# Optimization experiments

Hardware: AMD Instinct MI355X
Metric: run time of the kernel (lower is better)

The kernel has to match this reference:

```python
import math
import jax, jax.numpy as jnp
import numpy as np

B, I, G, C, D = 8192, 512, 32, 16, 32  # batch, dim_input, groups, num_components, dim_output
CD = C * D


def setup_inputs() -> dict:
    key = jax.random.key(0)
    ks = jax.random.split(key, 8)
    bound = 1.0 / math.sqrt(I)

    def unif(k, shape):
        return jax.random.uniform(k, shape, jnp.float32, -bound, bound)

    x = jax.random.normal(ks[0], (B, I), jnp.float32)
    # soft group-mixture weights (rows sum to 1, as produced upstream)
    g = jax.nn.softmax(jax.random.normal(ks[1], (B, G), jnp.float32), axis=-1)
    return {
        "x": x,
        "g": g,
        "W_mu": unif(ks[2], (G, I, CD)),
        "b_mu": unif(ks[3], (G, CD)),
        "W_sigma": unif(ks[4], (G, I, CD)),
        "b_sigma": unif(ks[5], (G, CD)),
        "W_pi": unif(ks[6], (G, I, C)),
        "b_pi": unif(ks[7], (G, C)),
    }


def _group_linear(x, g, W, b):
    # Fused form of: w_b = (g @ W.reshape(G, I*O)).reshape(B, I, O); x[:,None,:] @ w_b + g @ b
    # einsum avoids materializing the [B, I, O] per-sample weight tensor.
    return jnp.einsum("bi,gio,bg->bo", x, W, g) + g @ b


def reference(x, g, W_mu, b_mu, W_sigma, b_sigma, W_pi, b_pi):
    logits = _group_linear(x, g, W_pi, b_pi)                      # [B, C]
    loc = _group_linear(x, g, W_mu, b_mu)                         # [B, C*D]
    scale = jax.nn.softplus(_group_linear(x, g, W_sigma, b_sigma)) + 1e-7  # [B, C*D]
    # GroupGMM returns a MixtureSameFamily parameterized by (logits, loc, scale);
    # we return the concatenated parameter tensor [B, C + 2*C*D].
    return jnp.concatenate([logits, loc, scale], axis=-1)
```

## Files before the change

### kernel.cpp

```cpp
#include <hip/hip_runtime.h>
#include <hip/hip_bf16.h>

#define BATCH 8192
#define IDIM  512
#define GDIM  32
#define NOUT  1040
#define NPAD  1152
#define KW    16384
#define BM    128
#define BN    128
#define KQ    128

typedef short bf16x8 __attribute__((ext_vector_type(8)));
typedef float floatx4 __attribute__((ext_vector_type(4)));

__device__ inline unsigned pk2(float a, float b) {
    union { __hip_bfloat162 h2; unsigned u; } cv;
    cv.h2 = __float22bfloat162_rn(float2{a, b});
    return cv.u;
}

__global__ void cvt_bf16(const float* __restrict__ s, unsigned short* __restrict__ d) {
    int t = blockIdx.x * 256 + threadIdx.x;
    const float4* sp = (const float4*)s + (size_t)t * 2;
    float4 a = sp[0], b = sp[1];
    uint4 p;
    p.x = pk2(a.x, a.y); p.y = pk2(a.z, a.w);
    p.z = pk2(b.x, b.y); p.w = pk2(b.z, b.w);
    *(uint4*)(d + (size_t)t * 8) = p;
}

__global__ void prep_wt(const float* __restrict__ Wmu, const float* __restrict__ Wsig,
                        const float* __restrict__ Wpi, unsigned short* __restrict__ Wt) {
    int n = blockIdx.y * 256 + threadIdx.x;
    if (n >= NPAD) return;
    int k0 = blockIdx.x * 8;
    float v[8];
#pragma unroll
    for (int j = 0; j < 8; ++j) {
        int k = k0 + j, gg = k >> 9, i = k & 511;
        float val = 0.0f;
        if (n < 16)         val = Wpi [(gg * 512 + i) * 16  + n];
        else if (n < 528)   val = Wmu [(gg * 512 + i) * 512 + (n - 16)];
        else if (n < NOUT)  val = Wsig[(gg * 512 + i) * 512 + (n - 528)];
        v[j] = val;
    }
    uint4 p;
    p.x = pk2(v[0], v[1]); p.y = pk2(v[2], v[3]);
    p.z = pk2(v[4], v[5]); p.w = pk2(v[6], v[7]);
    const int col = n >> 7, r = n & 127;
    const int h = r >> 6, tn = (r >> 4) & 3, l15 = r & 15;
    const int kk = k0 >> 5, q = (k0 >> 3) & 3;
    size_t idx = ((size_t)(col * 512 + kk) << 12) + ((((h * 4 + tn) * 4 + q) * 16 + l15) * 8);
    *(uint4*)&Wt[idx] = p;
}

__global__ void prep_wb(const float* __restrict__ bmu, const float* __restrict__ bsig,
                        const float* __restrict__ bpi, unsigned short* __restrict__ Wb) {
    int n = blockIdx.y * 256 + threadIdx.x;
    if (n >= NPAD) return;
    int k0 = blockIdx.x * 8;
    float v[8];
#pragma unroll
    for (int j = 0; j < 8; ++j) {
        int gg = k0 + j;
        float val = 0.0f;
        if (n < 16)         val = bpi [gg * 16  + n];
        else if (n < 528)   val = bmu [gg * 512 + (n - 16)];
        else if (n < NOUT)  val = bsig[gg * 512 + (n - 528)];
        v[j] = val;
    }
    uint4 p;
    p.x = pk2(v[0], v[1]); p.y = pk2(v[2], v[3]);
    p.z = pk2(v[4], v[5]); p.w = pk2(v[6], v[7]);
    *(uint4*)&Wb[(size_t)n * GDIM + k0] = p;
}

__global__ __launch_bounds__(256, 2) void gemm_gmm(
        const unsigned short* __restrict__ xb, const unsigned short* __restrict__ gb,
        const float* __restrict__ g, const unsigned short* __restrict__ Wt,
        const unsigned short* __restrict__ Wb, float* __restrict__ out) {
    __shared__ unsigned short lA[BM * KQ];
    __shared__ float ratL[GDIM * BM];
    __shared__ float g31L[BM];

    const int t = threadIdx.x, lane = t & 63, w = t >> 6;
    const int wm = (w & 1) * 64, wn = (w >> 1) * 64;
    const int q = lane >> 4, l15 = lane & 15;

    const int bx = blockIdx.x;
    const int seq = (bx & 7) * 72 + (bx >> 3);
    const int col = seq >> 6, mblk = seq & 63;
    const int m0 = mblk * BM, n0 = col * BN;

    const unsigned short* Bbase = Wt + ((size_t)col * 512 << 12)
                                + (((wn >> 6) * 256 + lane) * 8);

    floatx4 acc[4][4] = {};
    uint4 breg[4][4];
    floatx4 r4[4];
    const int swA = l15 & 7;

    auto loadB = [&](int kk, int slot) {
        const unsigned kg = (((kk >> 2) & 31) * 16) + ((kk >> 7) * 4) + (kk & 3);
        const unsigned short* p = Bbase + ((size_t)kg << 12);
#pragma unroll
        for (int tn = 0; tn < 4; ++tn)
            breg[slot][tn] = *(const uint4*)(p + tn * 512);
    };
    auto loadR = [&](int gg) {
#pragma unroll
        for (int tm = 0; tm < 4; ++tm)
            r4[tm] = *(const floatx4*)&ratL[gg * BM + wm + tm * 16 + q * 4];
    };

    loadB(0, 0); loadB(1, 1); loadB(2, 2);

#pragma unroll
    for (int j = 0; j < 16; ++j) {
        int idx = t + 256 * j;
        int gg = idx >> 7, row = idx & 127;
        float cur  = g[(size_t)(m0 + row) * GDIM + gg];
        float prev = g[(size_t)(m0 + row) * GDIM + ((gg + 31) & 31)];
        ratL[idx] = prev / cur;
    }
    if (t < BM) g31L[t] = g[(size_t)(m0 + t) * GDIM + 31];
    __syncthreads();
    loadR(0);

    for (int kb = 0; kb < 4; ++kb) {
        __syncthreads();
        {
            const int r = t >> 1;
            const unsigned short* src = xb + (size_t)(m0 + r) * IDIM + kb * KQ + (t & 1) * 64;
#pragma unroll
            for (int j = 0; j < 8; ++j) {
                int gi = (t & 1) * 8 + j;
                uint4 v = *(const uint4*)(src + j * 8);
                *(uint4*)&lA[(r * 16 + (gi ^ (r & 7))) * 8] = v;
            }
        }
        __syncthreads();

        for (int gg = 0; gg < GDIM; ++gg) {
#pragma unroll
            for (int tm = 0; tm < 4; ++tm)
#pragma unroll
                for (int tn = 0; tn < 4; ++tn)
#pragma unroll
                    for (int r = 0; r < 4; ++r)
                        acc[tm][tn][r] *= r4[tm][r];
            loadR((gg + 1) & 31);

#pragma unroll
            for (int ks = 0; ks < 4; ++ks) {
                const int kk = ((kb * GDIM + gg) << 2) + ks;
                if (kk + 3 < 512) loadB(kk + 3, (ks + 3) & 3);
                bf16x8 af[4];
#pragma unroll
                for (int tm = 0; tm < 4; ++tm)
                    af[tm] = *(const bf16x8*)
                        &lA[((wm + tm * 16 + l15) * 16 + ((ks * 4 + q) ^ swA)) * 8];
#pragma unroll
                for (int tm = 0; tm < 4; ++tm)
#pragma unroll
                    for (int tn = 0; tn < 4; ++tn)
                        acc[tm][tn] = __builtin_amdgcn_mfma_f32_16x16x32_bf16(
                            af[tm], *(const bf16x8*)&breg[ks][tn], acc[tm][tn], 0, 0, 0);
            }
        }
    }

#pragma unroll
    for (int tm = 0; tm < 4; ++tm) {
        floatx4 gl = *(const floatx4*)&g31L[wm + tm * 16 + q * 4];
#pragma unroll
        for (int tn = 0; tn < 4; ++tn)
#pragma unroll
            for (int r = 0; r < 4; ++r)
                acc[tm][tn][r] *= gl[r];
    }

    __syncthreads();
    {
        const int r = t >> 1;
        const unsigned short* src = gb + (size_t)(m0 + r) * GDIM + (t & 1) * 16;
        *(uint4*)&lA[r * 40 + (t & 1) * 16]     = *(const uint4*)(src);
        *(uint4*)&lA[r * 40 + (t & 1) * 16 + 8] = *(const uint4*)(src + 8);
    }
    __syncthreads();
    {
        bf16x8 afb[4], bb[4];
#pragma unroll
        for (int tm = 0; tm < 4; ++tm)
            afb[tm] = *(const bf16x8*)&lA[(wm + tm * 16 + l15) * 40 + q * 8];
#pragma unroll
        for (int tn = 0; tn < 4; ++tn)
            bb[tn] = *(const bf16x8*)(Wb + (size_t)(n0 + wn + tn * 16 + l15) * GDIM + q * 8);
#pragma unroll
        for (int tm = 0; tm < 4; ++tm)
#pragma unroll
            for (int tn = 0; tn < 4; ++tn)
                acc[tm][tn] = __builtin_amdgcn_mfma_f32_16x16x32_bf16(
                    afb[tm], bb[tn], acc[tm][tn], 0, 0, 0);
    }

#pragma unroll
    for (int tn = 0; tn < 4; ++tn) {
        int n = n0 + wn + tn * 16 + l15;
        if (n >= NOUT) continue;
        bool is_scale = (n >= 528);
#pragma unroll
        for (int tm = 0; tm < 4; ++tm) {
            int mbase = m0 + wm + tm * 16 + q * 4;
#pragma unroll
            for (int r = 0; r < 4; ++r) {
                float vv = acc[tm][tn][r];
                if (is_scale) {
                    float sp = (vv > 15.0f) ? vv : log1pf(expf(vv));
                    vv = sp + 1e-7f;
                }
                out[(size_t)(mbase + r) * NOUT + n] = vv;
            }
        }
    }
}

extern "C" void kernel_launch(void* const* d_in, const int* in_sizes, int n_in,
                              void* d_out, int out_size, void* d_ws, size_t ws_size,
                              hipStream_t stream) {
    const float* x    = (const float*)d_in[0];
    const float* g    = (const float*)d_in[1];
    const float* Wmu  = (const float*)d_in[2];
    const float* bmu  = (const float*)d_in[3];
    const float* Wsig = (const float*)d_in[4];
    const float* bsig = (const float*)d_in[5];
    const float* Wpi  = (const float*)d_in[6];
    const float* bpi  = (const float*)d_in[7];
    float* out = (float*)d_out;

    char* ws = (char*)d_ws;
    unsigned short* Wt = (unsigned short*)ws;  ws += (size_t)NPAD * KW * 2;
    unsigned short* xb = (unsigned short*)ws;  ws += (size_t)BATCH * IDIM * 2;
    unsigned short* gb = (unsigned short*)ws;  ws += (size_t)BATCH * GDIM * 2;
    unsigned short* Wb = (unsigned short*)ws;

    cvt_bf16<<<BATCH * IDIM / 2048, 256, 0, stream>>>(x, xb);
    cvt_bf16<<<BATCH * GDIM / 2048, 256, 0, stream>>>(g, gb);
    prep_wt<<<dim3(KW / 8, 5), 256, 0, stream>>>(Wmu, Wsig, Wpi, Wt);
    prep_wb<<<dim3(GDIM / 8, 5), 256, 0, stream>>>(bmu, bsig, bpi, Wb);
    gemm_gmm<<<(BATCH / BM) * (NPAD / BN), 256, 0, stream>>>(xb, gb, g, Wt, Wb, out);
}
```

Measured before the change: 509.0 us.

## Hoist A fragments out of group loop and prefetch B per column

The A-operand fragments for all four k-steps are now loaded from LDS once per kb block into registers, instead of being reloaded every group iteration, so the same x tile is reused across all 32 groups. The B prefetch changes from a three-slot rolling buffer indexed by k-step to a per-column scheme: after each column's MFMAs finish, the next group's B fragments for that column are loaded. This removes repeated LDS reads but holds 16 more vector registers for A. The B prefetch distance also shrinks to within one group, which may expose global load latency or raise register pressure.

```diff
diff --git a/kernel.cpp b/kernel.cpp
--- a/kernel.cpp
+++ b/kernel.cpp
@@ -98,15 +98,16 @@
 
     floatx4 acc[4][4] = {};
     uint4 breg[4][4];
+    bf16x8 af[4][4];
     floatx4 r4[4];
     const int swA = l15 & 7;
 
-    auto loadB = [&](int kk, int slot) {
-        const unsigned kg = (((kk >> 2) & 31) * 16) + ((kk >> 7) * 4) + (kk & 3);
-        const unsigned short* p = Bbase + ((size_t)kg << 12);
-#pragma unroll
-        for (int tn = 0; tn < 4; ++tn)
-            breg[slot][tn] = *(const uint4*)(p + tn * 512);
+    auto loadBcol = [&](int flat, int tn) {
+        const int ggv = flat & 31, kbv = flat >> 5;
+        const unsigned short* p = Bbase + ((size_t)(ggv * 16 + kbv * 4) << 12) + tn * 512;
+#pragma unroll
+        for (int ks = 0; ks < 4; ++ks)
+            breg[ks][tn] = *(const uint4*)(p + (ks << 12));
     };
     auto loadR = [&](int gg) {
 #pragma unroll
@@ -114,7 +115,8 @@
             r4[tm] = *(const floatx4*)&ratL[gg * BM + wm + tm * 16 + q * 4];
     };
 
-    loadB(0, 0); loadB(1, 1); loadB(2, 2);
+#pragma unroll
+    for (int tn = 0; tn < 4; ++tn) loadBcol(0, tn);
 
 #pragma unroll
     for (int j = 0; j < 16; ++j) {
@@ -142,32 +144,30 @@
         }
         __syncthreads();
 
+#pragma unroll
+        for (int ks = 0; ks < 4; ++ks)
+#pragma unroll
+            for (int tm = 0; tm < 4; ++tm)
+                af[ks][tm] = *(const bf16x8*)
+                    &lA[((wm + tm * 16 + l15) * 16 + ((ks * 4 + q) ^ swA)) * 8];
+
         for (int gg = 0; gg < GDIM; ++gg) {
-#pragma unroll
-            for (int tm = 0; tm < 4; ++tm)
-#pragma unroll
-                for (int tn = 0; tn < 4; ++tn)
+            const int flat = kb * GDIM + gg;
+#pragma unroll
+            for (int tn = 0; tn < 4; ++tn) {
+#pragma unroll
+                for (int tm = 0; tm < 4; ++tm) {
 #pragma unroll
                     for (int r = 0; r < 4; ++r)
                         acc[tm][tn][r] *= r4[tm][r];
+#pragma unroll
+                    for (int ks = 0; ks < 4; ++ks)
+                        acc[tm][tn] = __builtin_amdgcn_mfma_f32_16x16x32_bf16(
+                            af[ks][tm], *(const bf16x8*)&breg[ks][tn], acc[tm][tn], 0, 0, 0);
+                }
+                if (flat + 1 < 128) loadBcol(flat + 1, tn);
+            }
             loadR((gg + 1) & 31);
-
-#pragma unroll
-            for (int ks = 0; ks < 4; ++ks) {
-                const int kk = ((kb * GDIM + gg) << 2) + ks;
-                if (kk + 3 < 512) loadB(kk + 3, (ks + 3) & 3);
-                bf16x8 af[4];
-#pragma unroll
-                for (int tm = 0; tm < 4; ++tm)
-                    af[tm] = *(const bf16x8*)
-                        &lA[((wm + tm * 16 + l15) * 16 + ((ks * 4 + q) ^ swA)) * 8];
-#pragma unroll
-                for (int tm = 0; tm < 4; ++tm)
-#pragma unroll
-                    for (int tn = 0; tn < 4; ++tn)
-                        acc[tm][tn] = __builtin_amdgcn_mfma_f32_16x16x32_bf16(
-                            af[tm], *(const bf16x8*)&breg[ks][tn], acc[tm][tn], 0, 0, 0);
-            }
         }
     }
 
```

Measured after the change: 493.0 us. 3.1% less time.

## Stage B tiles through LDS with async global_load_lds double buffering

Applied to the files above, without the earlier changes.

Replaces per-warp register prefetch of B fragments from global memory with a block-wide double-buffered LDS staging path using global_load_lds. Each k-step copies the B tile once per block instead of once per wave, and the A fragments for a K chunk are hoisted into registers once and reused across all groups. This adds two block barriers and explicit vmcnt/lgkmcnt waits per k-step, which may serialize waves and limit latency hiding.

```diff
diff --git a/kernel.cpp b/kernel.cpp
--- a/kernel.cpp
+++ b/kernel.cpp
@@ -14,6 +14,9 @@
 typedef short bf16x8 __attribute__((ext_vector_type(8)));
 typedef float floatx4 __attribute__((ext_vector_type(4)));
 
+typedef const __attribute__((address_space(1))) unsigned short gus_t;
+typedef __attribute__((address_space(3))) unsigned short lus_t;
+
 __device__ inline unsigned pk2(float a, float b) {
     union { __hip_bfloat162 h2; unsigned u; } cv;
     cv.h2 = __float22bfloat162_rn(float2{a, b});
@@ -81,11 +84,13 @@
         const float* __restrict__ g, const unsigned short* __restrict__ Wt,
         const unsigned short* __restrict__ Wb, float* __restrict__ out) {
     __shared__ unsigned short lA[BM * KQ];
+    __shared__ unsigned short bufB[2 * 4096];
     __shared__ float ratL[GDIM * BM];
     __shared__ float g31L[BM];
 
     const int t = threadIdx.x, lane = t & 63, w = t >> 6;
     const int wm = (w & 1) * 64, wn = (w >> 1) * 64;
+    const int h = w >> 1;
     const int q = lane >> 4, l15 = lane & 15;
 
     const int bx = blockIdx.x;
@@ -93,20 +98,19 @@
     const int col = seq >> 6, mblk = seq & 63;
     const int m0 = mblk * BM, n0 = col * BN;
 
-    const unsigned short* Bbase = Wt + ((size_t)col * 512 << 12)
-                                + (((wn >> 6) * 256 + lane) * 8);
+    const unsigned short* WtCol = Wt + ((size_t)col * 512 << 12);
 
     floatx4 acc[4][4] = {};
-    uint4 breg[4][4];
+    bf16x8 af[4][4];
     floatx4 r4[4];
     const int swA = l15 & 7;
 
-    auto loadB = [&](int kk, int slot) {
-        const unsigned kg = (((kk >> 2) & 31) * 16) + ((kk >> 7) * 4) + (kk & 3);
-        const unsigned short* p = Bbase + ((size_t)kg << 12);
-#pragma unroll
-        for (int tn = 0; tn < 4; ++tn)
-            breg[slot][tn] = *(const uint4*)(p + tn * 512);
+    auto stageB = [&](int s, int p) {
+        const int kg = (((s >> 2) & 31) << 4) + ((s >> 7) << 2) + (s & 3);
+        const unsigned short* src = WtCol + ((size_t)kg << 12) + t * 8;
+        unsigned short* dst = &bufB[p * 4096 + t * 8];
+        __builtin_amdgcn_global_load_lds((gus_t*)src,        (lus_t*)dst,        16, 0, 0);
+        __builtin_amdgcn_global_load_lds((gus_t*)(src+2048), (lus_t*)(dst+2048), 16, 0, 0);
     };
     auto loadR = [&](int gg) {
 #pragma unroll
@@ -114,7 +118,7 @@
             r4[tm] = *(const floatx4*)&ratL[gg * BM + wm + tm * 16 + q * 4];
     };
 
-    loadB(0, 0); loadB(1, 1); loadB(2, 2);
+    stageB(0, 0); stageB(1, 1);
 
 #pragma unroll
     for (int j = 0; j < 16; ++j) {
@@ -142,7 +146,18 @@
         }
         __syncthreads();
 
+#pragma unroll
+        for (int ks = 0; ks < 4; ++ks)
+#pragma unroll
+            for (int tm = 0; tm < 4; ++tm)
+                af[ks][tm] = *(const bf16x8*)
+                    &lA[((wm + tm * 16 + l15) * 16 + ((ks * 4 + q) ^ swA)) * 8];
+
         for (int gg = 0; gg < GDIM; ++gg) {
+            const int flat = kb * GDIM + gg;
+            const int sbase = flat * 4;
+            const bool lastgg = (kb == 3) && (gg == 31);
+
 #pragma unroll
             for (int tm = 0; tm < 4; ++tm)
 #pragma unroll
@@ -150,24 +165,36 @@
 #pragma unroll
                     for (int r = 0; r < 4; ++r)
                         acc[tm][tn][r] *= r4[tm][r];
-            loadR((gg + 1) & 31);
 
 #pragma unroll
             for (int ks = 0; ks < 4; ++ks) {
-                const int kk = ((kb * GDIM + gg) << 2) + ks;
-                if (kk + 3 < 512) loadB(kk + 3, (ks + 3) & 3);
-                bf16x8 af[4];
-#pragma unroll
-                for (int tm = 0; tm < 4; ++tm)
-                    af[tm] = *(const bf16x8*)
-                        &lA[((wm + tm * 16 + l15) * 16 + ((ks * 4 + q) ^ swA)) * 8];
+                const int p = ks & 1;
+                if (ks == 3) { if (lastgg) asm volatile("s_waitcnt vmcnt(0)" ::: "memory");
+                               else        asm volatile("s_waitcnt vmcnt(2)" ::: "memory"); }
+                else                       asm volatile("s_waitcnt vmcnt(2)" ::: "memory");
+                __builtin_amdgcn_sched_barrier(0);
+                __builtin_amdgcn_s_barrier();
+
+                bf16x8 bfr[4];
+#pragma unroll
+                for (int tn = 0; tn < 4; ++tn)
+                    bfr[tn] = *(const bf16x8*)
+                        &bufB[p * 4096 + (((h * 4 + tn) * 4 + q) * 16 + l15) * 8];
+                asm volatile("s_waitcnt lgkmcnt(0)" ::: "memory");
+                __builtin_amdgcn_sched_barrier(0);
+                __builtin_amdgcn_s_barrier();
+
+                const int s2 = sbase + ks + 2;
+                if (s2 < 512) stageB(s2, p);
+
 #pragma unroll
                 for (int tm = 0; tm < 4; ++tm)
 #pragma unroll
                     for (int tn = 0; tn < 4; ++tn)
                         acc[tm][tn] = __builtin_amdgcn_mfma_f32_16x16x32_bf16(
-                            af[tm], *(const bf16x8*)&breg[ks][tn], acc[tm][tn], 0, 0, 0);
+                            af[ks][tm], bfr[tn], acc[tm][tn], 0, 0, 0);
             }
+            loadR((gg + 1) & 31);
         }
     }
 
```

New measurement: 588.6 us. +15.7%, slower.
